# Kernel optimization log

Hardware: AMD Instinct MI355X
Metric: run time of the kernel (lower is better)

The kernel has to match this reference:

```python
import jax, jax.numpy as jnp
import numpy as np

N_HEADS = 16
D_KV = 64
NUM_BUCKETS = 32
MAX_DISTANCE = 128


def _relative_position_bucket(rel_pos, bidirectional=True, num_buckets=NUM_BUCKETS, max_distance=MAX_DISTANCE):
    # rel_pos: int32 [q, k] = key_pos - query_pos
    if bidirectional:
        num_buckets //= 2
        buckets = (rel_pos > 0).astype(jnp.int32) * num_buckets
        rel = jnp.abs(rel_pos)
    else:
        buckets = jnp.zeros_like(rel_pos)
        rel = -jnp.minimum(rel_pos, 0)
    max_exact = num_buckets // 2
    is_small = rel < max_exact
    # log-spaced buckets for large distances (guard log(0) with max(rel,1))
    rel_f = jnp.maximum(rel, 1).astype(jnp.float32)
    large = max_exact + (
        jnp.log(rel_f / max_exact) / np.log(max_distance / max_exact) * (num_buckets - max_exact)
    ).astype(jnp.int32)
    large = jnp.minimum(large, num_buckets - 1)
    return buckets + jnp.where(is_small, rel, large)


def compute_position_bias(rel_bias, q_len, k_len, bidirectional=True):
    # rel_bias: [num_buckets, n_heads] embedding table
    ctx = jnp.arange(q_len, dtype=jnp.int32)[:, None]
    mem = jnp.arange(k_len, dtype=jnp.int32)[None, :]
    buckets = _relative_position_bucket(mem - ctx, bidirectional=bidirectional)  # [q, k]
    values = rel_bias[buckets]                       # [q, k, h]
    return jnp.transpose(values, (2, 0, 1))[None]    # [1, h, q, k]


def setup_inputs() -> dict:
    key = jax.random.key(0)
    ks = jax.random.split(key, 6)
    B, S, D = 4, 1024, 1024
    scale = 0.02
    return {
        "hidden_states": jax.random.normal(ks[0], (B, S, D), jnp.float32),
        "attention_mask": jnp.zeros((1, 1, S, S), jnp.float32),
        "wq": jax.random.normal(ks[1], (D, D), jnp.float32) * scale,
        "wk": jax.random.normal(ks[2], (D, D), jnp.float32) * scale,
        "wv": jax.random.normal(ks[3], (D, D), jnp.float32) * scale,
        "wo": jax.random.normal(ks[4], (D, D), jnp.float32) * scale,
        "rel_bias": jax.random.normal(ks[5], (NUM_BUCKETS, N_HEADS), jnp.float32) * scale,
    }


def reference(hidden_states, attention_mask, wq, wk, wv, wo, rel_bias):
    B, S, D = hidden_states.shape
    H, dk = N_HEADS, D_KV

    def split_heads(x):  # [B, S, H*dk] -> [B, H, S, dk]
        return x.reshape(B, S, H, dk).transpose(0, 2, 1, 3)

    q = split_heads(hidden_states @ wq)
    k = split_heads(hidden_states @ wk)
    v = split_heads(hidden_states @ wv)

    # T5 attention: NO 1/sqrt(dk) scaling
    scores = jnp.einsum("bhqd,bhkd->bhqk", q, k)
    position_bias = compute_position_bias(rel_bias, S, S, bidirectional=True)
    position_bias = position_bias + attention_mask  # additive mask folded into bias
    scores = scores + position_bias

    attn = jax.nn.softmax(scores.astype(jnp.float32), axis=-1).astype(scores.dtype)
    out = jnp.einsum("bhqk,bhkd->bhqd", attn, v)
    out = out.transpose(0, 2, 1, 3).reshape(B, S, H * dk)
    return out @ wo
```

## Files before the change

kernel.cpp:

```cpp
#include <hip/hip_runtime.h>

typedef __attribute__((ext_vector_type(8))) short short8v;
typedef __attribute__((ext_vector_type(4))) short short4v;
typedef __attribute__((ext_vector_type(4))) float floatx4;
typedef __attribute__((ext_vector_type(16))) float f32x16;
typedef __attribute__((ext_vector_type(4))) unsigned uint4v;
typedef __attribute__((ext_vector_type(2))) unsigned uint2v;

#define S_LEN 1024
#define DMODEL 1024
#define NH 16
#define DK 64
#define NB_TAB 2047
#define L2E 1.4426950408889634f
#define FMAX_C 16.0f

__device__ __forceinline__ short f2bf(float f) {
  unsigned u = __builtin_bit_cast(unsigned, f);
  u += 0x7fffu + ((u >> 16) & 1u);
  return (short)(u >> 16);
}

__device__ __forceinline__ float b2f(short s) {
  return __builtin_bit_cast(float, ((unsigned)(unsigned short)s) << 16);
}

__device__ __forceinline__ unsigned cvtpk(float lo, float hi) {
  unsigned r;
  asm("v_cvt_pk_bf16_f32 %0, %1, %2" : "=v"(r) : "v"(lo), "v"(hi));
  return r;
}

__device__ __forceinline__ void pswap(unsigned& x, unsigned& y) {
  asm volatile("v_permlane32_swap_b32 %0, %1" : "+v"(x), "+v"(y));
}

__device__ __forceinline__ float exp2a(float x) {
  float r;
  asm("v_exp_f32 %0, %1" : "=v"(r) : "v"(x));
  return r;
}

__device__ __forceinline__ void load16(const void* g, void* l) {
  __builtin_amdgcn_global_load_lds((const __attribute__((address_space(1))) unsigned*)g,
                                   (__attribute__((address_space(3))) unsigned*)l, 16, 0, 0);
}

__global__ __launch_bounds__(256) void transpose4_k(const float* __restrict__ wq,
                                                    const float* __restrict__ wk,
                                                    const float* __restrict__ wv,
                                                    const float* __restrict__ wo,
                                                    short* __restrict__ wT,
                                                    short* __restrict__ wTo) {
  __shared__ float t[32][33];
  int z = blockIdx.z;
  const float* in = z == 0 ? wq : (z == 1 ? wk : (z == 2 ? wv : wo));
  short* out = z < 3 ? wT + (size_t)z * 1024 * 1024 : wTo;
  int tx = threadIdx.x, ty = threadIdx.y;
  int bx = blockIdx.x * 32, by = blockIdx.y * 32;
#pragma unroll
  for (int i = ty; i < 32; i += 8) t[i][tx] = in[(size_t)(by + i) * DMODEL + bx + tx];
  __syncthreads();
#pragma unroll
  for (int i = ty; i < 32; i += 8) out[(size_t)(bx + i) * DMODEL + by + tx] = f2bf(t[tx][i]);
}

__global__ __launch_bounds__(256) void cvt_k(const float* __restrict__ in,
                                             short* __restrict__ out) {
  size_t i = ((size_t)blockIdx.x * 256 + threadIdx.x) * 8;
  const floatx4* p = (const floatx4*)(in + i);
  floatx4 a = p[0], b = p[1];
  short8v o;
#pragma unroll
  for (int j = 0; j < 4; ++j) {
    o[j] = f2bf(a[j]);
    o[4 + j] = f2bf(b[j]);
  }
  *(short8v*)(out + i) = o;
}

__global__ __launch_bounds__(256) void bias4_k(const float* __restrict__ rel_bias,
                                               short* __restrict__ B4) {
  int gid = blockIdx.x * 256 + threadIdx.x;
  int h = gid >> 11, idx = gid & 2047;
  short4v o;
#pragma unroll
  for (int j = 0; j < 4; ++j) {
    int ri = idx + j;
    if (ri > 2046) ri = 2046;
    int rel = ri - 1023;
    int bucket = (rel > 0) ? 16 : 0;
    int r = rel < 0 ? -rel : rel;
    int bb;
    if (r < 8) {
      bb = r;
    } else {
      float lf = logf((float)r * 0.125f) * (8.0f / 2.772588722239781f);
      bb = 8 + (int)lf;
      if (bb > 15) bb = 15;
    }
    bucket += bb;
    o[j] = f2bf(rel_bias[bucket * NH + h] * L2E);
  }
  *(short4v*)(B4 + (size_t)gid * 4) = o;
}

__global__ __launch_bounds__(256) void masksw_k(const float* __restrict__ mask,
                                                short* __restrict__ Msw) {
  int gid = blockIdx.x * 256 + threadIdx.x;
  int q = gid >> 7, kvg = gid & 127;
  int kv = kvg * 8;
  floatx4 m0 = *(const floatx4*)(mask + (size_t)q * 1024 + kv);
  floatx4 m1 = *(const floatx4*)(mask + (size_t)q * 1024 + kv + 4);
  unsigned u0 = cvtpk(m0[0] * L2E - FMAX_C, m0[1] * L2E - FMAX_C);
  unsigned u1 = cvtpk(m0[2] * L2E - FMAX_C, m0[3] * L2E - FMAX_C);
  unsigned u2 = cvtpk(m1[0] * L2E - FMAX_C, m1[1] * L2E - FMAX_C);
  unsigned u3 = cvtpk(m1[2] * L2E - FMAX_C, m1[3] * L2E - FMAX_C);
  uint4v uu;
  if (q & 8) {
    uu[0] = u2; uu[1] = u3; uu[2] = u0; uu[3] = u1;
  } else {
    uu[0] = u0; uu[1] = u1; uu[2] = u2; uu[3] = u3;
  }
  int seg = kvg >> 3, sslot = (kvg & 7) ^ (q & 7);
  *(uint4v*)(Msw + (size_t)q * 1024 + seg * 64 + sslot * 8) = uu;
}

__global__ __launch_bounds__(256) void vtrans_k(const short* __restrict__ V,
                                                short* __restrict__ Vt) {
  __shared__ short t[64 * 256];
  int tid = threadIdx.x;
  int s0 = blockIdx.x * 256;
  int bh = blockIdx.y;
#pragma unroll
  for (int i = 0; i < 8; ++i) {
    int s = i * 32 + (tid >> 3);
    int slot = tid & 7;
    short8v vv = *(const short8v*)&V[(((size_t)bh * S_LEN) + s0 + s) * DK + slot * 8];
#pragma unroll
    for (int j = 0; j < 8; ++j) {
      int d = slot * 8 + j;
      *(short*)((char*)t + d * 512 + ((s * 2) ^ (((d >> 3) & 7) << 4))) = vv[j];
    }
  }
  __syncthreads();
#pragma unroll
  for (int i = 0; i < 8; ++i) {
    int d = i * 8 + (tid >> 5);
    int sl = tid & 31;
    short8v vv = *(const short8v*)((char*)t + d * 512 + ((sl * 16) ^ (((d >> 3) & 7) << 4)));
    *(short8v*)&Vt[(((size_t)bh * DK) + d) * S_LEN + s0 + sl * 8] = vv;
  }
}

template <int EPI, int NBN, int NBM>
__global__ __launch_bounds__(256) void gemm2_k(const short* __restrict__ A,
                                               const short* __restrict__ BT,
                                               short* __restrict__ Qo, short* __restrict__ Ko,
                                               short* __restrict__ Vo, float* __restrict__ Fo) {
  constexpr int K = DMODEL;
  constexpr int TOTAL = NBN * NBM;
  constexpr int CHUNK = TOTAL / 8;
  __shared__ short lA[128 * 64];
  __shared__ short lB[128 * 64];
  int tid = threadIdx.x;
  int lane = tid & 63, wid = tid >> 6;
  int lane16 = lane & 15, kl = lane >> 4;
  int bid = blockIdx.x;
  int lb = (bid & 7) * CHUNK + (bid >> 3);
  int g = lb / (8 * NBN), r = lb % (8 * NBN);
  int bm = (g * 8 + (r & 7)) * 128, bn = (r >> 3) * 128;
  int wm = (wid & 1) * 64, wn = (wid >> 1) * 64;
  floatx4 acc[4][4] = {};

  const char* gA[4];
  const char* gB[4];
  int slot = lane & 7;
#pragma unroll
  for (int it = 0; it < 4; ++it) {
    int row = it * 32 + wid * 8 + (lane >> 3);
    int sw = (slot * 16) ^ ((row & 7) << 4);
    gA[it] = (const char*)A + ((size_t)(bm + row) * K) * 2 + sw;
    gB[it] = (const char*)BT + ((size_t)(bn + row) * K) * 2 + sw;
  }

  for (int k0 = 0; k0 < K; k0 += 64) {
    __syncthreads();
#pragma unroll
    for (int it = 0; it < 4; ++it) {
      char* la = (char*)lA + (it * 32 + wid * 8) * 128;
      char* lb2 = (char*)lB + (it * 32 + wid * 8) * 128;
      load16(gA[it] + k0 * 2, la);
      load16(gB[it] + k0 * 2, lb2);
    }
    __syncthreads();
#pragma unroll
    for (int kc = 0; kc < 2; ++kc) {
      short8v af[4], bf[4];
#pragma unroll
      for (int mt = 0; mt < 4; ++mt) {
        int row = wm + mt * 16 + lane16;
        af[mt] = *(const short8v*)((char*)lA + row * 128 +
                                   ((kc * 64 + kl * 16) ^ ((row & 7) << 4)));
      }
#pragma unroll
      for (int nt = 0; nt < 4; ++nt) {
        int row = wn + nt * 16 + lane16;
        bf[nt] = *(const short8v*)((char*)lB + row * 128 +
                                   ((kc * 64 + kl * 16) ^ ((row & 7) << 4)));
      }
#pragma unroll
      for (int mt = 0; mt < 4; ++mt)
#pragma unroll
        for (int nt = 0; nt < 4; ++nt)
          acc[mt][nt] =
              __builtin_amdgcn_mfma_f32_16x16x32_bf16(af[mt], bf[nt], acc[mt][nt], 0, 0, 0);
    }
  }
  if constexpr (EPI == 0) {
    int which = bn >> 10;
    int gcb = bn & 1023;
    short* dst = which == 0 ? Qo : (which == 1 ? Ko : Vo);
    float scl = which == 0 ? L2E : 1.0f;
#pragma unroll
    for (int mt = 0; mt < 4; ++mt)
#pragma unroll
      for (int nt = 0; nt < 4; ++nt)
#pragma unroll
        for (int r2 = 0; r2 < 4; ++r2) {
          int gr = bm + wm + mt * 16 + kl * 4 + r2;
          int gc = gcb + wn + nt * 16 + lane16;
          int hh = gc >> 6, d = gc & 63;
          int bb = gr >> 10, s = gr & 1023;
          dst[(size_t)((bb * 16 + hh) * 1024 + s) * 64 + d] = f2bf(acc[mt][nt][r2] * scl);
        }
  } else {
#pragma unroll
    for (int mt = 0; mt < 4; ++mt)
#pragma unroll
      for (int nt = 0; nt < 4; ++nt)
#pragma unroll
        for (int r2 = 0; r2 < 4; ++r2) {
          int gr = bm + wm + mt * 16 + kl * 4 + r2;
          int gc = bn + wn + nt * 16 + lane16;
          Fo[(size_t)gr * DMODEL + gc] = acc[mt][nt][r2];
        }
  }
}

__global__ __launch_bounds__(256) void attn32_k(const short* __restrict__ Q,
                                                const short* __restrict__ Kg,
                                                const short* __restrict__ Vt,
                                                const short* __restrict__ Msw,
                                                const short* __restrict__ B4g,
                                                short* __restrict__ O) {
  __shared__ short lK[2][64 * 64];
  __shared__ short lV[2][64 * 64];
  __shared__ short lM[2][128 * 64];
  __shared__ short lB4[2048 * 4];
  int tid = threadIdx.x;
  int lane = tid & 63, wid = tid >> 6;
  int l31 = lane & 31, L = lane >> 5;
  int bid = blockIdx.x;
  int lb = (bid & 7) * 64 + (bid >> 3);
  int bh = lb >> 3, qt = lb & 7;
  int h = bh & 15, b = bh >> 4;
  int q = qt * 128 + wid * 32 + l31;
  int q_r = wid * 32 + l31;

  const char* gK[2];
  const char* gV[2];
  int ldst[2];
  {
    int slot = lane & 7;
#pragma unroll
    for (int i = 0; i < 2; ++i) {
      int row = i * 32 + wid * 8 + (lane >> 3);
      int ss = slot ^ ((row ^ (row >> 3)) & 7);
      gK[i] = (const char*)Kg + ((size_t)(bh * S_LEN + row) * DK + ss * 8) * 2;
      gV[i] = (const char*)Vt + ((size_t)(bh * DK + row) * S_LEN + ss * 8) * 2;
      ldst[i] = (i * 32 + wid * 8) * 128;
    }
  }
  const char* gM[4];
  int ldstM[4];
#pragma unroll
  for (int c = 0; c < 4; ++c) {
    int row = c * 32 + wid * 8 + (lane >> 3);
    gM[c] = (const char*)Msw + ((size_t)(qt * 128 + row) * 1024) * 2 + (lane & 7) * 16;
    ldstM[c] = c * 4096 + wid * 1024;
  }
#pragma unroll
  for (int i = 0; i < 2; ++i) {
    load16(gK[i], (char*)lK[0] + ldst[i]);
    load16(gV[i], (char*)lV[0] + ldst[i]);
  }
#pragma unroll
  for (int c = 0; c < 4; ++c) load16(gM[c], (char*)lM[0] + ldstM[c]);
  {
    const short8v* src = (const short8v*)(B4g + (size_t)h * 8192);
    short8v* dst = (short8v*)lB4;
    for (int i = tid; i < 1024; i += 256) dst[i] = src[i];
  }
  const short8v* qp = (const short8v*)(Q + ((size_t)bh * S_LEN + q) * DK);
  short8v qf[4];
#pragma unroll
  for (int ds = 0; ds < 4; ++ds) qf[ds] = qp[ds * 2 + L];

  f32x16 ot[2] = {};
  float l_ = 0.0f;
  int swq = ((q_r & 7) << 4) | (q_r & 8);
  __syncthreads();

  for (int it = 0; it < 16; ++it) {
    int kv0 = it * 64;
    int cur = it & 1;
    if (it < 15) {
#pragma unroll
      for (int i = 0; i < 2; ++i) {
        load16(gK[i] + (size_t)(kv0 + 64) * 128, (char*)lK[cur ^ 1] + ldst[i]);
        load16(gV[i] + (size_t)(kv0 + 64) * 2, (char*)lV[cur ^ 1] + ldst[i]);
      }
#pragma unroll
      for (int c = 0; c < 4; ++c)
        load16(gM[c] + (size_t)(kv0 + 64) * 2, (char*)lM[cur ^ 1] + ldstM[c]);
    }
    short4v mb[2][4], bb[2][4];
#pragma unroll
    for (int hh = 0; hh < 2; ++hh)
#pragma unroll
      for (int g = 0; g < 4; ++g) {
        mb[hh][g] = *(const short4v*)((const char*)lM[cur] + q_r * 128 +
                                      ((hh * 64 + 16 * g + 8 * L) ^ swq));
        bb[hh][g] =
            *(const short4v*)(lB4 + (size_t)(kv0 + hh * 32 + 8 * g + 4 * L - q + 1023) * 4);
      }
    f32x16 sA[2];
#pragma unroll
    for (int hh = 0; hh < 2; ++hh) {
      f32x16 acc = {};
#pragma unroll
      for (int ds = 0; ds < 4; ++ds) {
        int row = hh * 32 + l31;
        int sw = ((row ^ (row >> 3)) & 7) << 4;
        short8v kf =
            *(const short8v*)((const char*)lK[cur] + row * 128 + ((ds * 32 + L * 16) ^ sw));
        acc = __builtin_amdgcn_mfma_f32_32x32x16_bf16(kf, qf[ds], acc, 0, 0, 0);
      }
      sA[hh] = acc;
    }
    float p[2][16];
#pragma unroll
    for (int hh = 0; hh < 2; ++hh)
#pragma unroll
      for (int g = 0; g < 4; ++g)
#pragma unroll
        for (int r3 = 0; r3 < 4; ++r3)
          p[hh][4 * g + r3] = sA[hh][4 * g + r3] + b2f(mb[hh][g][r3]) + b2f(bb[hh][g][r3]);
    float s0 = 0.0f, s1 = 0.0f, s2 = 0.0f, s3 = 0.0f;
#pragma unroll
    for (int hh = 0; hh < 2; ++hh)
#pragma unroll
      for (int g = 0; g < 4; ++g) {
        float e0 = exp2a(p[hh][4 * g + 0]);
        float e1 = exp2a(p[hh][4 * g + 1]);
        float e2 = exp2a(p[hh][4 * g + 2]);
        float e3 = exp2a(p[hh][4 * g + 3]);
        p[hh][4 * g + 0] = e0;
        p[hh][4 * g + 1] = e1;
        p[hh][4 * g + 2] = e2;
        p[hh][4 * g + 3] = e3;
        s0 += e0;
        s1 += e1;
        s2 += e2;
        s3 += e3;
      }
    l_ += (s0 + s1) + (s2 + s3);
#pragma unroll
    for (int ks = 0; ks < 4; ++ks) {
      const int hh = ks >> 1, bq = (ks & 1) * 8;
      unsigned A0 = cvtpk(p[hh][bq + 0], p[hh][bq + 1]);
      unsigned A1 = cvtpk(p[hh][bq + 2], p[hh][bq + 3]);
      unsigned B0 = cvtpk(p[hh][bq + 4], p[hh][bq + 5]);
      unsigned B1 = cvtpk(p[hh][bq + 6], p[hh][bq + 7]);
      pswap(A0, B0);
      pswap(A1, B1);
      uint4v uu = {A0, A1, B0, B1};
      short8v pf = __builtin_bit_cast(short8v, uu);
#pragma unroll
      for (int dt = 0; dt < 2; ++dt) {
        int row = dt * 32 + l31;
        int sw = ((row ^ (row >> 3)) & 7) << 4;
        short8v vf =
            *(const short8v*)((const char*)lV[cur] + row * 128 + ((ks * 32 + L * 16) ^ sw));
        ot[dt] = __builtin_amdgcn_mfma_f32_32x32x16_bf16(vf, pf, ot[dt], 0, 0, 0);
      }
    }
    __syncthreads();
  }
  l_ += __shfl_xor(l_, 32);
  float inv = 1.0f / l_;
  short* ob = O + ((size_t)(b * S_LEN + q)) * DMODEL + h * 64;
#pragma unroll
  for (int dt = 0; dt < 2; ++dt)
#pragma unroll
    for (int g = 0; g < 4; ++g) {
      int d0 = dt * 32 + 8 * g + 4 * L;
      uint2v w = {cvtpk(ot[dt][4 * g + 0] * inv, ot[dt][4 * g + 1] * inv),
                  cvtpk(ot[dt][4 * g + 2] * inv, ot[dt][4 * g + 3] * inv)};
      *(uint2v*)(ob + d0) = w;
    }
}

extern "C" void kernel_launch(void* const* d_in, const int* in_sizes, int n_in, void* d_out,
                              int out_size, void* d_ws, size_t ws_size, hipStream_t stream) {
  (void)in_sizes;
  (void)n_in;
  (void)out_size;
  (void)ws_size;
  const float* hs = (const float*)d_in[0];
  const float* mask = (const float*)d_in[1];
  const float* wq = (const float*)d_in[2];
  const float* wk = (const float*)d_in[3];
  const float* wv = (const float*)d_in[4];
  const float* wo = (const float*)d_in[5];
  const float* relb = (const float*)d_in[6];
  float* out = (float*)d_out;
  char* ws = (char*)d_ws;
  const size_t MB = 1024 * 1024;
  short* wT = (short*)(ws);
  short* wTo = (short*)(ws + 6 * MB);
  short* Ab = (short*)(ws + 8 * MB);
  short* Qb = (short*)(ws + 16 * MB);
  short* Kb = (short*)(ws + 24 * MB);
  short* Vb = (short*)(ws + 32 * MB);
  short* Vtb = (short*)(ws + 40 * MB);
  short* B4 = (short*)(ws + 48 * MB);
  short* Msw = (short*)(ws + 49 * MB);
  short* Ob = Ab;

  transpose4_k<<<dim3(32, 32, 4), dim3(32, 8), 0, stream>>>(wq, wk, wv, wo, wT, wTo);
  bias4_k<<<16 * 2048 / 256, 256, 0, stream>>>(relb, B4);
  masksw_k<<<1024 * 128 / 256, 256, 0, stream>>>(mask, Msw);
  cvt_k<<<4096 * 1024 / 8 / 256, 256, 0, stream>>>(hs, Ab);
  gemm2_k<0, 24, 32><<<768, 256, 0, stream>>>(Ab, wT, Qb, Kb, Vb, nullptr);
  vtrans_k<<<dim3(4, 64), 256, 0, stream>>>(Vb, Vtb);
  attn32_k<<<512, 256, 0, stream>>>(Qb, Kb, Vtb, Msw, B4, Ob);
  gemm2_k<1, 8, 32><<<256, 256, 0, stream>>>(Ob, wTo, nullptr, nullptr, nullptr, out);
}
```

Measured before the change: 195.7 us.

## Merge prep kernels, fuse V transpose into QKV GEMM, double-buffer GEMMs

The four preprocessing kernels (weight transpose, hidden-state conversion, mask swizzle, bias table) become one launch that dispatches on block index. The QKV GEMM now writes V directly in a transposed, pre-swizzled layout, so the separate vtrans kernel is gone and the attention V load no longer applies its own swizzle. Both GEMMs switch to double-buffered LDS with 32-wide K sub-tiles to overlap global loads with MFMA work. The output GEMM uses 128x64 tiles with 512 blocks instead of 256. Together these aim to cut launch overhead, one V round trip, and load latency, at the cost of more complex indexing and a new swizzle contract between the QKV GEMM and attention.

```diff
diff --git a/kernel.cpp b/kernel.cpp
--- a/kernel.cpp
+++ b/kernel.cpp
@@ -46,181 +46,158 @@
                                    (__attribute__((address_space(3))) unsigned*)l, 16, 0, 0);
 }
 
-__global__ __launch_bounds__(256) void transpose4_k(const float* __restrict__ wq,
-                                                    const float* __restrict__ wk,
-                                                    const float* __restrict__ wv,
-                                                    const float* __restrict__ wo,
-                                                    short* __restrict__ wT,
-                                                    short* __restrict__ wTo) {
+__global__ __launch_bounds__(256) void prep_k(const float* __restrict__ hs,
+                                              const float* __restrict__ mask,
+                                              const float* __restrict__ wq,
+                                              const float* __restrict__ wk,
+                                              const float* __restrict__ wv,
+                                              const float* __restrict__ wo,
+                                              const float* __restrict__ relb,
+                                              short* __restrict__ wT, short* __restrict__ wTo,
+                                              short* __restrict__ Ab, short* __restrict__ Msw,
+                                              short* __restrict__ B4) {
   __shared__ float t[32][33];
-  int z = blockIdx.z;
-  const float* in = z == 0 ? wq : (z == 1 ? wk : (z == 2 ? wv : wo));
-  short* out = z < 3 ? wT + (size_t)z * 1024 * 1024 : wTo;
-  int tx = threadIdx.x, ty = threadIdx.y;
-  int bx = blockIdx.x * 32, by = blockIdx.y * 32;
-#pragma unroll
-  for (int i = ty; i < 32; i += 8) t[i][tx] = in[(size_t)(by + i) * DMODEL + bx + tx];
-  __syncthreads();
-#pragma unroll
-  for (int i = ty; i < 32; i += 8) out[(size_t)(bx + i) * DMODEL + by + tx] = f2bf(t[tx][i]);
-}
-
-__global__ __launch_bounds__(256) void cvt_k(const float* __restrict__ in,
-                                             short* __restrict__ out) {
-  size_t i = ((size_t)blockIdx.x * 256 + threadIdx.x) * 8;
-  const floatx4* p = (const floatx4*)(in + i);
-  floatx4 a = p[0], b = p[1];
-  short8v o;
-#pragma unroll
-  for (int j = 0; j < 4; ++j) {
-    o[j] = f2bf(a[j]);
-    o[4 + j] = f2bf(b[j]);
-  }
-  *(short8v*)(out + i) = o;
-}
-
-__global__ __launch_bounds__(256) void bias4_k(const float* __restrict__ rel_bias,
-                                               short* __restrict__ B4) {
-  int gid = blockIdx.x * 256 + threadIdx.x;
-  int h = gid >> 11, idx = gid & 2047;
-  short4v o;
-#pragma unroll
-  for (int j = 0; j < 4; ++j) {
-    int ri = idx + j;
-    if (ri > 2046) ri = 2046;
-    int rel = ri - 1023;
-    int bucket = (rel > 0) ? 16 : 0;
-    int r = rel < 0 ? -rel : rel;
-    int bb;
-    if (r < 8) {
-      bb = r;
+  int bid = blockIdx.x, tid = threadIdx.x;
+  if (bid < 4096) {
+    int z = bid >> 10, tb = bid & 1023;
+    const float* in = z == 0 ? wq : (z == 1 ? wk : (z == 2 ? wv : wo));
+    short* out = z < 3 ? wT + (size_t)z * 1024 * 1024 : wTo;
+    int tx = tid & 31, ty = tid >> 5;
+    int bx = (tb & 31) * 32, by = (tb >> 5) * 32;
+#pragma unroll
+    for (int i = ty; i < 32; i += 8) t[i][tx] = in[(size_t)(by + i) * DMODEL + bx + tx];
+    __syncthreads();
+#pragma unroll
+    for (int i = ty; i < 32; i += 8) out[(size_t)(bx + i) * DMODEL + by + tx] = f2bf(t[tx][i]);
+  } else if (bid < 6144) {
+    size_t i = ((size_t)(bid - 4096) * 256 + tid) * 8;
+    const floatx4* p = (const floatx4*)(hs + i);
+    floatx4 a = p[0], b = p[1];
+    short8v o;
+#pragma unroll
+    for (int j = 0; j < 4; ++j) {
+      o[j] = f2bf(a[j]);
+      o[4 + j] = f2bf(b[j]);
+    }
+    *(short8v*)(Ab + i) = o;
+  } else if (bid < 6656) {
+    int gid = (bid - 6144) * 256 + tid;
+    int q = gid >> 7, kvg = gid & 127;
+    int kv = kvg * 8;
+    floatx4 m0 = *(const floatx4*)(mask + (size_t)q * 1024 + kv);
+    floatx4 m1 = *(const floatx4*)(mask + (size_t)q * 1024 + kv + 4);
+    unsigned u0 = cvtpk(m0[0] * L2E - FMAX_C, m0[1] * L2E - FMAX_C);
+    unsigned u1 = cvtpk(m0[2] * L2E - FMAX_C, m0[3] * L2E - FMAX_C);
+    unsigned u2 = cvtpk(m1[0] * L2E - FMAX_C, m1[1] * L2E - FMAX_C);
+    unsigned u3 = cvtpk(m1[2] * L2E - FMAX_C, m1[3] * L2E - FMAX_C);
+    uint4v uu;
+    if (q & 8) {
+      uu[0] = u2; uu[1] = u3; uu[2] = u0; uu[3] = u1;
     } else {
-      float lf = logf((float)r * 0.125f) * (8.0f / 2.772588722239781f);
-      bb = 8 + (int)lf;
-      if (bb > 15) bb = 15;
-    }
-    bucket += bb;
-    o[j] = f2bf(rel_bias[bucket * NH + h] * L2E);
-  }
-  *(short4v*)(B4 + (size_t)gid * 4) = o;
-}
-
-__global__ __launch_bounds__(256) void masksw_k(const float* __restrict__ mask,
-                                                short* __restrict__ Msw) {
-  int gid = blockIdx.x * 256 + threadIdx.x;
-  int q = gid >> 7, kvg = gid & 127;
-  int kv = kvg * 8;
-  floatx4 m0 = *(const floatx4*)(mask + (size_t)q * 1024 + kv);
-  floatx4 m1 = *(const floatx4*)(mask + (size_t)q * 1024 + kv + 4);
-  unsigned u0 = cvtpk(m0[0] * L2E - FMAX_C, m0[1] * L2E - FMAX_C);
-  unsigned u1 = cvtpk(m0[2] * L2E - FMAX_C, m0[3] * L2E - FMAX_C);
-  unsigned u2 = cvtpk(m1[0] * L2E - FMAX_C, m1[1] * L2E - FMAX_C);
-  unsigned u3 = cvtpk(m1[2] * L2E - FMAX_C, m1[3] * L2E - FMAX_C);
-  uint4v uu;
-  if (q & 8) {
-    uu[0] = u2; uu[1] = u3; uu[2] = u0; uu[3] = u1;
+      uu[0] = u0; uu[1] = u1; uu[2] = u2; uu[3] = u3;
+    }
+    int seg = kvg >> 3, sslot = (kvg & 7) ^ (q & 7);
+    *(uint4v*)(Msw + (size_t)q * 1024 + seg * 64 + sslot * 8) = uu;
   } else {
-    uu[0] = u0; uu[1] = u1; uu[2] = u2; uu[3] = u3;
-  }
-  int seg = kvg >> 3, sslot = (kvg & 7) ^ (q & 7);
-  *(uint4v*)(Msw + (size_t)q * 1024 + seg * 64 + sslot * 8) = uu;
-}
-
-__global__ __launch_bounds__(256) void vtrans_k(const short* __restrict__ V,
-                                                short* __restrict__ Vt) {
-  __shared__ short t[64 * 256];
-  int tid = threadIdx.x;
-  int s0 = blockIdx.x * 256;
-  int bh = blockIdx.y;
-#pragma unroll
-  for (int i = 0; i < 8; ++i) {
-    int s = i * 32 + (tid >> 3);
-    int slot = tid & 7;
-    short8v vv = *(const short8v*)&V[(((size_t)bh * S_LEN) + s0 + s) * DK + slot * 8];
-#pragma unroll
-    for (int j = 0; j < 8; ++j) {
-      int d = slot * 8 + j;
-      *(short*)((char*)t + d * 512 + ((s * 2) ^ (((d >> 3) & 7) << 4))) = vv[j];
-    }
-  }
-  __syncthreads();
-#pragma unroll
-  for (int i = 0; i < 8; ++i) {
-    int d = i * 8 + (tid >> 5);
-    int sl = tid & 31;
-    short8v vv = *(const short8v*)((char*)t + d * 512 + ((sl * 16) ^ (((d >> 3) & 7) << 4)));
-    *(short8v*)&Vt[(((size_t)bh * DK) + d) * S_LEN + s0 + sl * 8] = vv;
-  }
-}
-
-template <int EPI, int NBN, int NBM>
-__global__ __launch_bounds__(256) void gemm2_k(const short* __restrict__ A,
-                                               const short* __restrict__ BT,
-                                               short* __restrict__ Qo, short* __restrict__ Ko,
-                                               short* __restrict__ Vo, float* __restrict__ Fo) {
+    int gid = (bid - 6656) * 256 + tid;
+    int h = gid >> 11, idx = gid & 2047;
+    short4v o;
+#pragma unroll
+    for (int j = 0; j < 4; ++j) {
+      int ri = idx + j;
+      if (ri > 2046) ri = 2046;
+      int rel = ri - 1023;
+      int bucket = (rel > 0) ? 16 : 0;
+      int r = rel < 0 ? -rel : rel;
+      int bb;
+      if (r < 8) {
+        bb = r;
+      } else {
+        float lf = logf((float)r * 0.125f) * (8.0f / 2.772588722239781f);
+        bb = 8 + (int)lf;
+        if (bb > 15) bb = 15;
+      }
+      bucket += bb;
+      o[j] = f2bf(relb[bucket * NH + h] * L2E);
+    }
+    *(short4v*)(B4 + (size_t)gid * 4) = o;
+  }
+}
+
+__global__ __launch_bounds__(256) void gemmQKV_k(const short* __restrict__ A,
+                                                 const short* __restrict__ BT,
+                                                 short* __restrict__ Qo, short* __restrict__ Ko,
+                                                 short* __restrict__ Vt) {
   constexpr int K = DMODEL;
-  constexpr int TOTAL = NBN * NBM;
-  constexpr int CHUNK = TOTAL / 8;
-  __shared__ short lA[128 * 64];
-  __shared__ short lB[128 * 64];
+  __shared__ short lA[2][128 * 32];
+  __shared__ short lB[2][128 * 32];
   int tid = threadIdx.x;
   int lane = tid & 63, wid = tid >> 6;
   int lane16 = lane & 15, kl = lane >> 4;
   int bid = blockIdx.x;
-  int lb = (bid & 7) * CHUNK + (bid >> 3);
-  int g = lb / (8 * NBN), r = lb % (8 * NBN);
+  int lb = (bid & 7) * 96 + (bid >> 3);
+  int g = lb / 192, r = lb % 192;
   int bm = (g * 8 + (r & 7)) * 128, bn = (r >> 3) * 128;
   int wm = (wid & 1) * 64, wn = (wid >> 1) * 64;
   floatx4 acc[4][4] = {};
 
-  const char* gA[4];
-  const char* gB[4];
-  int slot = lane & 7;
-#pragma unroll
-  for (int it = 0; it < 4; ++it) {
-    int row = it * 32 + wid * 8 + (lane >> 3);
-    int sw = (slot * 16) ^ ((row & 7) << 4);
-    gA[it] = (const char*)A + ((size_t)(bm + row) * K) * 2 + sw;
-    gB[it] = (const char*)BT + ((size_t)(bn + row) * K) * 2 + sw;
-  }
-
-  for (int k0 = 0; k0 < K; k0 += 64) {
+  const char* gA[2];
+  const char* gB[2];
+  int ldstS[2];
+  {
+    int slot = lane & 3;
+#pragma unroll
+    for (int it = 0; it < 2; ++it) {
+      int row = it * 64 + wid * 16 + (lane >> 2);
+      int ss = slot ^ ((row ^ (row >> 2)) & 3);
+      gA[it] = (const char*)A + ((size_t)(bm + row) * K + ss * 8) * 2;
+      gB[it] = (const char*)BT + ((size_t)(bn + row) * K + ss * 8) * 2;
+      ldstS[it] = it * 4096 + wid * 1024;
+    }
+  }
+#pragma unroll
+  for (int it = 0; it < 2; ++it) {
+    load16(gA[it], (char*)lA[0] + ldstS[it]);
+    load16(gB[it], (char*)lB[0] + ldstS[it]);
+  }
+  __syncthreads();
+
+  for (int t = 0; t < 32; ++t) {
+    int cur = t & 1;
+    if (t < 31) {
+      int kb = (t + 1) * 64;
+#pragma unroll
+      for (int it = 0; it < 2; ++it) {
+        load16(gA[it] + kb, (char*)lA[cur ^ 1] + ldstS[it]);
+        load16(gB[it] + kb, (char*)lB[cur ^ 1] + ldstS[it]);
+      }
+    }
+    short8v af[4], bf[4];
+#pragma unroll
+    for (int mt = 0; mt < 4; ++mt) {
+      int row = wm + mt * 16 + lane16;
+      int k2 = ((row ^ (row >> 2)) & 3) << 4;
+      af[mt] = *(const short8v*)((char*)lA[cur] + row * 64 + ((kl * 16) ^ k2));
+    }
+#pragma unroll
+    for (int nt = 0; nt < 4; ++nt) {
+      int row = wn + nt * 16 + lane16;
+      int k2 = ((row ^ (row >> 2)) & 3) << 4;
+      bf[nt] = *(const short8v*)((char*)lB[cur] + row * 64 + ((kl * 16) ^ k2));
+    }
+#pragma unroll
+    for (int mt = 0; mt < 4; ++mt)
+#pragma unroll
+      for (int nt = 0; nt < 4; ++nt)
+        acc[mt][nt] =
+            __builtin_amdgcn_mfma_f32_16x16x32_bf16(af[mt], bf[nt], acc[mt][nt], 0, 0, 0);
     __syncthreads();
-#pragma unroll
-    for (int it = 0; it < 4; ++it) {
-      char* la = (char*)lA + (it * 32 + wid * 8) * 128;
-      char* lb2 = (char*)lB + (it * 32 + wid * 8) * 128;
-      load16(gA[it] + k0 * 2, la);
-      load16(gB[it] + k0 * 2, lb2);
-    }
-    __syncthreads();
-#pragma unroll
-    for (int kc = 0; kc < 2; ++kc) {
-      short8v af[4], bf[4];
-#pragma unroll
-      for (int mt = 0; mt < 4; ++mt) {
-        int row = wm + mt * 16 + lane16;
-        af[mt] = *(const short8v*)((char*)lA + row * 128 +
-                                   ((kc * 64 + kl * 16) ^ ((row & 7) << 4)));
-      }
-#pragma unroll
-      for (int nt = 0; nt < 4; ++nt) {
-        int row = wn + nt * 16 + lane16;
-        bf[nt] = *(const short8v*)((char*)lB + row * 128 +
-                                   ((kc * 64 + kl * 16) ^ ((row & 7) << 4)));
-      }
-#pragma unroll
-      for (int mt = 0; mt < 4; ++mt)
-#pragma unroll
-        for (int nt = 0; nt < 4; ++nt)
-          acc[mt][nt] =
-              __builtin_amdgcn_mfma_f32_16x16x32_bf16(af[mt], bf[nt], acc[mt][nt], 0, 0, 0);
-    }
-  }
-  if constexpr (EPI == 0) {
-    int which = bn >> 10;
-    int gcb = bn & 1023;
-    short* dst = which == 0 ? Qo : (which == 1 ? Ko : Vo);
+  }
+
+  int which = bn >> 10;
+  int gcb = bn & 1023;
+  if (which < 2) {
+    short* dst = which == 0 ? Qo : Ko;
     float scl = which == 0 ? L2E : 1.0f;
 #pragma unroll
     for (int mt = 0; mt < 4; ++mt)
@@ -238,14 +215,98 @@
 #pragma unroll
     for (int mt = 0; mt < 4; ++mt)
 #pragma unroll
-      for (int nt = 0; nt < 4; ++nt)
-#pragma unroll
-        for (int r2 = 0; r2 < 4; ++r2) {
-          int gr = bm + wm + mt * 16 + kl * 4 + r2;
-          int gc = bn + wn + nt * 16 + lane16;
-          Fo[(size_t)gr * DMODEL + gc] = acc[mt][nt][r2];
-        }
-  }
+      for (int nt = 0; nt < 4; ++nt) {
+        int sb = bm + wm + mt * 16 + kl * 4;
+        int gc = gcb + wn + nt * 16 + lane16;
+        int hh = gc >> 6, d = gc & 63;
+        int bb = sb >> 10, st = sb & 1023;
+        int keyd = (d ^ (d >> 3)) & 7;
+        size_t off = ((size_t)((bb * 16 + hh) * 64 + d)) * 1024 + (st & ~63) +
+                     ((((st >> 3) & 7) ^ keyd) << 3) + (st & 7);
+        short4v o;
+#pragma unroll
+        for (int r2 = 0; r2 < 4; ++r2) o[r2] = f2bf(acc[mt][nt][r2]);
+        *(short4v*)(Vt + off) = o;
+      }
+  }
+}
+
+__global__ __launch_bounds__(256) void gemmO_k(const short* __restrict__ A,
+                                               const short* __restrict__ BT,
+                                               float* __restrict__ Fo) {
+  constexpr int K = DMODEL;
+  __shared__ short lA[2][128 * 32];
+  __shared__ short lB[2][64 * 32];
+  int tid = threadIdx.x;
+  int lane = tid & 63, wid = tid >> 6;
+  int lane16 = lane & 15, kl = lane >> 4;
+  int bid = blockIdx.x;
+  int lb = (bid & 7) * 64 + (bid >> 3);
+  int g = lb / 128, r = lb % 128;
+  int bm = (g * 8 + (r & 7)) * 128, bn = (r >> 3) * 64;
+  int wm = (wid & 1) * 64, wn = (wid >> 1) * 32;
+  floatx4 acc[4][2] = {};
+
+  const char* gA[2];
+  const char* gB;
+  int ldstS[2];
+  {
+    int slot = lane & 3;
+#pragma unroll
+    for (int it = 0; it < 2; ++it) {
+      int row = it * 64 + wid * 16 + (lane >> 2);
+      int ss = slot ^ ((row ^ (row >> 2)) & 3);
+      gA[it] = (const char*)A + ((size_t)(bm + row) * K + ss * 8) * 2;
+      ldstS[it] = it * 4096 + wid * 1024;
+    }
+    int row = wid * 16 + (lane >> 2);
+    int ss = slot ^ ((row ^ (row >> 2)) & 3);
+    gB = (const char*)BT + ((size_t)(bn + row) * K + ss * 8) * 2;
+  }
+#pragma unroll
+  for (int it = 0; it < 2; ++it) load16(gA[it], (char*)lA[0] + ldstS[it]);
+  load16(gB, (char*)lB[0] + ldstS[0]);
+  __syncthreads();
+
+  for (int t = 0; t < 32; ++t) {
+    int cur = t & 1;
+    if (t < 31) {
+      int kb = (t + 1) * 64;
+#pragma unroll
+      for (int it = 0; it < 2; ++it) load16(gA[it] + kb, (char*)lA[cur ^ 1] + ldstS[it]);
+      load16(gB + kb, (char*)lB[cur ^ 1] + ldstS[0]);
+    }
+    short8v af[4], bf[2];
+#pragma unroll
+    for (int mt = 0; mt < 4; ++mt) {
+      int row = wm + mt * 16 + lane16;
+      int k2 = ((row ^ (row >> 2)) & 3) << 4;
+      af[mt] = *(const short8v*)((char*)lA[cur] + row * 64 + ((kl * 16) ^ k2));
+    }
+#pragma unroll
+    for (int nt = 0; nt < 2; ++nt) {
+      int row = wn + nt * 16 + lane16;
+      int k2 = ((row ^ (row >> 2)) & 3) << 4;
+      bf[nt] = *(const short8v*)((char*)lB[cur] + row * 64 + ((kl * 16) ^ k2));
+    }
+#pragma unroll
+    for (int mt = 0; mt < 4; ++mt)
+#pragma unroll
+      for (int nt = 0; nt < 2; ++nt)
+        acc[mt][nt] =
+            __builtin_amdgcn_mfma_f32_16x16x32_bf16(af[mt], bf[nt], acc[mt][nt], 0, 0, 0);
+    __syncthreads();
+  }
+#pragma unroll
+  for (int mt = 0; mt < 4; ++mt)
+#pragma unroll
+    for (int nt = 0; nt < 2; ++nt)
+#pragma unroll
+      for (int r2 = 0; r2 < 4; ++r2) {
+        int gr = bm + wm + mt * 16 + kl * 4 + r2;
+        int gc = bn + wn + nt * 16 + lane16;
+        Fo[(size_t)gr * DMODEL + gc] = acc[mt][nt][r2];
+      }
 }
 
 __global__ __launch_bounds__(256) void attn32_k(const short* __restrict__ Q,
@@ -278,7 +339,7 @@
       int row = i * 32 + wid * 8 + (lane >> 3);
       int ss = slot ^ ((row ^ (row >> 3)) & 7);
       gK[i] = (const char*)Kg + ((size_t)(bh * S_LEN + row) * DK + ss * 8) * 2;
-      gV[i] = (const char*)Vt + ((size_t)(bh * DK + row) * S_LEN + ss * 8) * 2;
+      gV[i] = (const char*)Vt + ((size_t)(bh * DK + row) * S_LEN + slot * 8) * 2;
       ldst[i] = (i * 32 + wid * 8) * 128;
     }
   }
@@ -329,11 +390,11 @@
 #pragma unroll
     for (int hh = 0; hh < 2; ++hh)
 #pragma unroll
-      for (int g = 0; g < 4; ++g) {
-        mb[hh][g] = *(const short4v*)((const char*)lM[cur] + q_r * 128 +
-                                      ((hh * 64 + 16 * g + 8 * L) ^ swq));
-        bb[hh][g] =
-            *(const short4v*)(lB4 + (size_t)(kv0 + hh * 32 + 8 * g + 4 * L - q + 1023) * 4);
+      for (int g2 = 0; g2 < 4; ++g2) {
+        mb[hh][g2] = *(const short4v*)((const char*)lM[cur] + q_r * 128 +
+                                       ((hh * 64 + 16 * g2 + 8 * L) ^ swq));
+        bb[hh][g2] =
+            *(const short4v*)(lB4 + (size_t)(kv0 + hh * 32 + 8 * g2 + 4 * L - q + 1023) * 4);
       }
     f32x16 sA[2];
 #pragma unroll
@@ -353,23 +414,23 @@
 #pragma unroll
     for (int hh = 0; hh < 2; ++hh)
 #pragma unroll
-      for (int g = 0; g < 4; ++g)
+      for (int g2 = 0; g2 < 4; ++g2)
 #pragma unroll
         for (int r3 = 0; r3 < 4; ++r3)
-          p[hh][4 * g + r3] = sA[hh][4 * g + r3] + b2f(mb[hh][g][r3]) + b2f(bb[hh][g][r3]);
+          p[hh][4 * g2 + r3] = sA[hh][4 * g2 + r3] + b2f(mb[hh][g2][r3]) + b2f(bb[hh][g2][r3]);
     float s0 = 0.0f, s1 = 0.0f, s2 = 0.0f, s3 = 0.0f;
 #pragma unroll
     for (int hh = 0; hh < 2; ++hh)
 #pragma unroll
-      for (int g = 0; g < 4; ++g) {
-        float e0 = exp2a(p[hh][4 * g + 0]);
-        float e1 = exp2a(p[hh][4 * g + 1]);
-        float e2 = exp2a(p[hh][4 * g + 2]);
-        float e3 = exp2a(p[hh][4 * g + 3]);
-        p[hh][4 * g + 0] = e0;
-        p[hh][4 * g + 1] = e1;
-        p[hh][4 * g + 2] = e2;
-        p[hh][4 * g + 3] = e3;
+      for (int g2 = 0; g2 < 4; ++g2) {
+        float e0 = exp2a(p[hh][4 * g2 + 0]);
+        float e1 = exp2a(p[hh][4 * g2 + 1]);
+        float e2 = exp2a(p[hh][4 * g2 + 2]);
+        float e3 = exp2a(p[hh][4 * g2 + 3]);
+        p[hh][4 * g2 + 0] = e0;
+        p[hh][4 * g2 + 1] = e1;
+        p[hh][4 * g2 + 2] = e2;
+        p[hh][4 * g2 + 3] = e3;
         s0 += e0;
         s1 += e1;
         s2 += e2;
@@ -404,10 +465,10 @@
 #pragma unroll
   for (int dt = 0; dt < 2; ++dt)
 #pragma unroll
-    for (int g = 0; g < 4; ++g) {
-      int d0 = dt * 32 + 8 * g + 4 * L;
-      uint2v w = {cvtpk(ot[dt][4 * g + 0] * inv, ot[dt][4 * g + 1] * inv),
-                  cvtpk(ot[dt][4 * g + 2] * inv, ot[dt][4 * g + 3] * inv)};
+    for (int g2 = 0; g2 < 4; ++g2) {
+      int d0 = dt * 32 + 8 * g2 + 4 * L;
+      uint2v w = {cvtpk(ot[dt][4 * g2 + 0] * inv, ot[dt][4 * g2 + 1] * inv),
+                  cvtpk(ot[dt][4 * g2 + 2] * inv, ot[dt][4 * g2 + 3] * inv)};
       *(uint2v*)(ob + d0) = w;
     }
 }
@@ -433,18 +494,13 @@
   short* Ab = (short*)(ws + 8 * MB);
   short* Qb = (short*)(ws + 16 * MB);
   short* Kb = (short*)(ws + 24 * MB);
-  short* Vb = (short*)(ws + 32 * MB);
-  short* Vtb = (short*)(ws + 40 * MB);
+  short* Vtb = (short*)(ws + 32 * MB);
   short* B4 = (short*)(ws + 48 * MB);
   short* Msw = (short*)(ws + 49 * MB);
   short* Ob = Ab;
 
-  transpose4_k<<<dim3(32, 32, 4), dim3(32, 8), 0, stream>>>(wq, wk, wv, wo, wT, wTo);
-  bias4_k<<<16 * 2048 / 256, 256, 0, stream>>>(relb, B4);
-  masksw_k<<<1024 * 128 / 256, 256, 0, stream>>>(mask, Msw);
-  cvt_k<<<4096 * 1024 / 8 / 256, 256, 0, stream>>>(hs, Ab);
-  gemm2_k<0, 24, 32><<<768, 256, 0, stream>>>(Ab, wT, Qb, Kb, Vb, nullptr);
-  vtrans_k<<<dim3(4, 64), 256, 0, stream>>>(Vb, Vtb);
+  prep_k<<<6784, 256, 0, stream>>>(hs, mask, wq, wk, wv, wo, relb, wT, wTo, Ab, Msw, B4);
+  gemmQKV_k<<<768, 256, 0, stream>>>(Ab, wT, Qb, Kb, Vtb);
   attn32_k<<<512, 256, 0, stream>>>(Qb, Kb, Vtb, Msw, B4, Ob);
-  gemm2_k<1, 8, 32><<<256, 256, 0, stream>>>(Ob, wTo, nullptr, nullptr, nullptr, out);
-}
+  gemmO_k<<<512, 256, 0, stream>>>(Ob, wTo, out);
+}
```

Result: faster. 180.7 us (-7.7%).
